# Optimization experiments

Hardware: AMD Instinct MI355X
Metric: run time of the kernel (lower is better)

Reference implementation:

```python
import jax, jax.numpy as jnp
import numpy as np

# Kernel offset table copied VERBATIM from the source (note the duplicated
# [-1,-1] row where [-1,1] would be expected -- we replicate the bug).
OFF = jnp.array([[-1, -1], [-1, 0], [-1, -1], [0, -1], [0, 0], [0, 1],
                 [1, -1], [1, 0], [1, 1]], dtype=jnp.float32)  # (9, 2)

T_HARD = 3.14 / 6
S_HARD = 2.0
S_RANGE = (S_HARD - 1.0 / S_HARD) / 2.0
H_VEC = jnp.array([T_HARD, S_RANGE, S_RANGE], dtype=jnp.float32)
B_VEC = jnp.array([0.0, S_RANGE, S_RANGE], dtype=jnp.float32)
BN_EPS = 1e-5


def setup_inputs() -> dict:
    key = jax.random.key(0)
    ks = jax.random.split(key, 9)
    N, C, H, W, O = 8, 128, 64, 64, 128
    return {
        "input_feat": jax.random.normal(ks[0], (N, C, H, W), jnp.float32),
        "ste_w": 0.05 * jax.random.normal(ks[1], (3, C, 1, 1), jnp.float32),
        "ste_b": 0.05 * jax.random.normal(ks[2], (3,), jnp.float32),
        "bn_gamma": 1.0 + 0.1 * jax.random.normal(ks[3], (3,), jnp.float32),
        "bn_beta": 0.1 * jax.random.normal(ks[4], (3,), jnp.float32),
        "bn_mean": 0.1 * jax.random.normal(ks[5], (3,), jnp.float32),
        "bn_var": jax.random.uniform(ks[6], (3,), jnp.float32, 0.5, 1.5),
        "dconv_w": jax.random.normal(ks[7], (O, C, 3, 3), jnp.float32) / np.sqrt(C * 9.0),
        "dconv_b": 0.05 * jax.random.normal(ks[8], (O,), jnp.float32),
    }


def _forward(input_feat, ste_w, ste_b, bn_gamma, bn_beta, bn_mean, bn_var,
             dconv_w, dconv_b):
    N, C, H, W = input_feat.shape
    O = dconv_w.shape[0]
    # --- ste: 1x1 conv -> BatchNorm (eval) -> tanh, then affine H*x + B ---
    s = jnp.einsum('nchw,oc->nohw', input_feat, ste_w[:, :, 0, 0])
    s = s + ste_b[None, :, None, None]
    scale = (bn_gamma / jnp.sqrt(bn_var + BN_EPS))
    s = (s - bn_mean[None, :, None, None]) * scale[None, :, None, None] \
        + bn_beta[None, :, None, None]
    info = jnp.tanh(s) * H_VEC[None, :, None, None] + B_VEC[None, :, None, None]
    # --- per-pixel 2x2 scaled rotation applied to kernel grid ---
    theta = info[:, 0]                  # [N,H,W]
    sin = jnp.sin(theta)
    cos = jnp.cos(theta)
    a00 = cos * info[:, 1]
    a11 = cos * info[:, 2]
    awt = jnp.stack([a00, -sin, sin, a11], axis=-1).reshape(N, H, W, 2, 2)
    offs = jnp.einsum('kd,nhwde->nkhwe', OFF, awt)   # [N,9,H,W,2]
    off_y = offs[..., 0]
    off_x = offs[..., 1]
    # --- deformable 3x3 conv, stride 1, padding 1, zero-pad bilinear ---
    k = jnp.arange(9)
    dy = (k // 3 - 1).astype(jnp.float32)  # default kernel y-offsets
    dx = (k % 3 - 1).astype(jnp.float32)
    yy = jnp.arange(H, dtype=jnp.float32)
    xx = jnp.arange(W, dtype=jnp.float32)
    y = yy[None, None, :, None] + dy[None, :, None, None] + off_y  # [N,9,H,W]
    x = xx[None, None, None, :] + dx[None, :, None, None] + off_x
    y0 = jnp.floor(y)
    x0 = jnp.floor(x)
    wy = y - y0
    wx = x - x0
    y0i = y0.astype(jnp.int32)
    x0i = x0.astype(jnp.int32)

    def gather(img, yi, xi):
        # img [C,H,W], yi/xi [9,H,W] -> [C,9,H,W], zero outside bounds
        valid = (yi >= 0) & (yi < H) & (xi >= 0) & (xi < W)
        v = img[:, jnp.clip(yi, 0, H - 1), jnp.clip(xi, 0, W - 1)]
        return v * valid[None].astype(img.dtype)

    def sample_one(img, y0i, x0i, wy, wx):
        v00 = gather(img, y0i, x0i)
        v01 = gather(img, y0i, x0i + 1)
        v10 = gather(img, y0i + 1, x0i)
        v11 = gather(img, y0i + 1, x0i + 1)
        return (v00 * ((1 - wy) * (1 - wx))[None]
                + v01 * ((1 - wy) * wx)[None]
                + v10 * (wy * (1 - wx))[None]
                + v11 * (wy * wx)[None])

    samp = jax.vmap(sample_one)(input_feat, y0i, x0i, wy, wx)  # [N,C,9,H,W]
    out = jnp.einsum('nckhw,ock->nohw', samp, dconv_w.reshape(O, C, 9))
    return out + dconv_b[None, :, None, None]


def reference(input_feat, ste_w, ste_b, bn_gamma, bn_beta, bn_mean, bn_var,
              dconv_w, dconv_b):
    return _forward(input_feat, ste_w, ste_b, bn_gamma, bn_beta, bn_mean,
                    bn_var, dconv_w, dconv_b)
```

## Files before the change

kernel.cpp:

```cpp
#include <hip/hip_runtime.h>

constexpr int kN = 8, kC = 128, kH = 64, kW = 64, kO = 128;
constexpr int kHW = kH * kW;

typedef float f32x4 __attribute__((ext_vector_type(4)));
typedef short bf16x8 __attribute__((ext_vector_type(8)));
typedef unsigned short ushort8 __attribute__((ext_vector_type(8)));

__device__ __forceinline__ float bf2f(unsigned short u) {
  unsigned int x = ((unsigned int)u) << 16;
  return __builtin_bit_cast(float, x);
}
__device__ __forceinline__ unsigned short f2bf(float f) {
  unsigned int b = __builtin_bit_cast(unsigned int, f);
  b += 0x7FFFu + ((b >> 16) & 1u);
  return (unsigned short)(b >> 16);
}

__global__ __launch_bounds__(256) void prep_kernel(
    const float* __restrict__ inp, const float* __restrict__ ste_w,
    const float* __restrict__ ste_b, const float* __restrict__ bn_g,
    const float* __restrict__ bn_b, const float* __restrict__ bn_m,
    const float* __restrict__ bn_v, unsigned short* __restrict__ nhwc,
    float* __restrict__ prm) {
  __shared__ float tile[kC * kW];
  __shared__ float part[4][3][kW];
  const int tid = threadIdx.x;
  const int nh = blockIdx.x;
  const int n = nh >> 6, h = nh & 63;
  const float* base = inp + (size_t)n * kC * kHW + h * kW;

  for (int i = tid; i < kC * kW; i += 256) {
    int c = i >> 6, w = i & 63;
    tile[i] = base[c * kHW + w];
  }
  __syncthreads();

  {
    const int w = tid & 63, cg = tid >> 6;
    float s0 = 0.f, s1 = 0.f, s2 = 0.f;
#pragma unroll 8
    for (int j = 0; j < 32; ++j) {
      int c = cg * 32 + j;
      float v = tile[c * kW + w];
      s0 += v * ste_w[c];
      s1 += v * ste_w[kC + c];
      s2 += v * ste_w[2 * kC + c];
    }
    part[cg][0][w] = s0;
    part[cg][1][w] = s1;
    part[cg][2][w] = s2;
  }
  __syncthreads();
  if (tid < kW) {
    const int w = tid;
    float s0 = part[0][0][w] + part[1][0][w] + part[2][0][w] + part[3][0][w];
    float s1 = part[0][1][w] + part[1][1][w] + part[2][1][w] + part[3][1][w];
    float s2 = part[0][2][w] + part[1][2][w] + part[2][2][w] + part[3][2][w];
    s0 = (s0 + ste_b[0] - bn_m[0]) * (bn_g[0] * rsqrtf(bn_v[0] + 1e-5f)) + bn_b[0];
    s1 = (s1 + ste_b[1] - bn_m[1]) * (bn_g[1] * rsqrtf(bn_v[1] + 1e-5f)) + bn_b[1];
    s2 = (s2 + ste_b[2] - bn_m[2]) * (bn_g[2] * rsqrtf(bn_v[2] + 1e-5f)) + bn_b[2];
    float th = tanhf(s0) * (3.14f / 6.0f);
    float i1 = tanhf(s1) * 0.75f + 0.75f;
    float i2 = tanhf(s2) * 0.75f + 0.75f;
    float sn = sinf(th), cs = cosf(th);
    prm[nh * 192 + w * 3 + 0] = cs * i1;
    prm[nh * 192 + w * 3 + 1] = sn;
    prm[nh * 192 + w * 3 + 2] = cs * i2;
  }

  for (int i = tid; i < kW * 16; i += 256) {
    int w = i & 63, ch = i >> 6;
    int c0 = ch * 8;
    ushort8 v;
#pragma unroll
    for (int j = 0; j < 8; ++j) v[j] = f2bf(tile[(c0 + j) * kW + w]);
    *(ushort8*)&nhwc[((size_t)(n * kH + h) * kW + w) * kC + c0] = v;
  }
}

__global__ __launch_bounds__(256) void reorder_bf16_kernel(
    const float* __restrict__ dw, unsigned short* __restrict__ wkb) {
  int idx = blockIdx.x * blockDim.x + threadIdx.x;
  if (idx >= 9 * kO * kC) return;
  int k = idx / (kO * kC);
  int r = idx - k * (kO * kC);
  int o = r >> 7, c = r & 127;
  wkb[idx] = f2bf(dw[(o * kC + c) * 9 + k]);
}

__global__ __launch_bounds__(512, 4) void deform_mfma_kernel(
    const unsigned short* __restrict__ nhwc,
    const unsigned short* __restrict__ wkb,
    const float* __restrict__ prm, const float* __restrict__ db,
    float* __restrict__ out) {
  __shared__ __align__(16) unsigned short As[2][32 * 128];
  __shared__ __align__(16) unsigned short Bs[2][128 * 128];

  const int tid = threadIdx.x;
  const int lane = tid & 63, wave = tid >> 6;
  const int nh = blockIdx.x >> 1;
  const int w0 = (blockIdx.x & 1) << 5;
  const int n = nh >> 6, h = nh & 63;
  const unsigned short* nhwc_n = nhwc + (size_t)n * kH * kW * kC;

  const int p = tid >> 4, ch = tid & 15;
  const float a00 = prm[nh * 192 + (w0 + p) * 3 + 0];
  const float sn  = prm[nh * 192 + (w0 + p) * 3 + 1];
  const float a11 = prm[nh * 192 + (w0 + p) * 3 + 2];

  const int mg = wave >> 2, ng = wave & 3;
  const int row = mg * 16 + (lane & 15);
  const int kq = lane >> 4;
  const int rsw = (row & 7) << 4;
  f32x4 acc[2];
  acc[0] = (f32x4){0.f, 0.f, 0.f, 0.f};
  acc[1] = (f32x4){0.f, 0.f, 0.f, 0.f};

  ushort8 bReg[4];
  ushort8 a00r, a01r, a10r, a11r;
  float w00, w01, w10, w11;

  auto issue_tap = [&](int k) {
    const unsigned short* wkp = wkb + (size_t)k * kO * kC;
#pragma unroll
    for (int it = 0; it < 4; ++it) {
      int i = tid + it * 512;
      int o = i >> 4, c8 = i & 15;
      bReg[it] = *(const ushort8*)&wkp[o * kC + c8 * 8];
    }
    const float fdy = (float)(k / 3 - 1);
    const float fdx = (float)(k % 3 - 1);
    const float o0 = fdy;
    const float o1 = (k == 2) ? -1.0f : fdx;
    float y = (float)h + fdy + o0 * a00 + o1 * sn;
    float x = (float)(w0 + p) + fdx - o0 * sn + o1 * a11;
    float y0f = floorf(y), x0f = floorf(x);
    float wy = y - y0f, wx = x - x0f;
    int y0 = (int)y0f, x0 = (int)x0f;
    bool yv0 = (unsigned)y0 < (unsigned)kH;
    bool yv1 = (unsigned)(y0 + 1) < (unsigned)kH;
    bool xv0 = (unsigned)x0 < (unsigned)kW;
    bool xv1 = (unsigned)(x0 + 1) < (unsigned)kW;
    int y0c = min(max(y0, 0), kH - 1);
    int y1c = min(max(y0 + 1, 0), kH - 1);
    int x0c = min(max(x0, 0), kW - 1);
    int x1c = min(max(x0 + 1, 0), kW - 1);
    w00 = (1.f - wy) * (1.f - wx) * (yv0 && xv0 ? 1.f : 0.f);
    w01 = (1.f - wy) * wx * (yv0 && xv1 ? 1.f : 0.f);
    w10 = wy * (1.f - wx) * (yv1 && xv0 ? 1.f : 0.f);
    w11 = wy * wx * (yv1 && xv1 ? 1.f : 0.f);
    const int cb = ch * 8;
    a00r = *(const ushort8*)&nhwc_n[((y0c * kW) + x0c) * kC + cb];
    a01r = *(const ushort8*)&nhwc_n[((y0c * kW) + x1c) * kC + cb];
    a10r = *(const ushort8*)&nhwc_n[((y1c * kW) + x0c) * kC + cb];
    a11r = *(const ushort8*)&nhwc_n[((y1c * kW) + x1c) * kC + cb];
  };

  auto write_tiles = [&](int buf) {
#pragma unroll
    for (int it = 0; it < 4; ++it) {
      int i = tid + it * 512;
      int o = i >> 4, c8 = i & 15;
      *(ushort8*)((char*)Bs[buf] + o * 256 + ((c8 * 16) ^ ((o & 7) << 4))) =
          bReg[it];
    }
    ushort8 r;
#pragma unroll
    for (int j = 0; j < 8; ++j) {
      float val = bf2f(a00r[j]) * w00 + bf2f(a01r[j]) * w01 +
                  bf2f(a10r[j]) * w10 + bf2f(a11r[j]) * w11;
      r[j] = f2bf(val);
    }
    *(ushort8*)((char*)As[buf] + p * 256 + ((ch * 16) ^ ((p & 7) << 4))) = r;
  };

  issue_tap(0);
  write_tiles(0);
  __syncthreads();

  for (int k = 0; k < 9; ++k) {
    const int cur = k & 1;
    if (k < 8) issue_tap(k + 1);

    const char* Ab = (const char*)As[cur];
    const char* Bb = (const char*)Bs[cur];
#pragma unroll
    for (int ks = 0; ks < 4; ++ks) {
      const int kb = ks * 64 + kq * 16;
      bf16x8 a = *(const bf16x8*)(Ab + row * 256 + (kb ^ rsw));
#pragma unroll
      for (int f = 0; f < 2; ++f) {
        const int orow = (ng * 2 + f) * 16 + (lane & 15);
        bf16x8 b = *(const bf16x8*)(Bb + orow * 256 + (kb ^ ((orow & 7) << 4)));
        acc[f] = __builtin_amdgcn_mfma_f32_16x16x32_bf16(a, b, acc[f], 0, 0, 0);
      }
    }

    if (k < 8) write_tiles(cur ^ 1);
    __syncthreads();
  }

  const int pixb = mg * 16 + (lane >> 4) * 4;
#pragma unroll
  for (int f = 0; f < 2; ++f) {
    const int o = (ng * 2 + f) * 16 + (lane & 15);
    const float bias = db[o];
    float4 v = {acc[f][0] + bias, acc[f][1] + bias, acc[f][2] + bias,
                acc[f][3] + bias};
    *(float4*)&out[((size_t)(n * kO + o)) * kHW + h * kW + w0 + pixb] = v;
  }
}

__global__ __launch_bounds__(256) void deform_kernel_f32(
    const float* __restrict__ inp, const float* __restrict__ ste_w,
    const float* __restrict__ ste_b, const float* __restrict__ bn_g,
    const float* __restrict__ bn_b, const float* __restrict__ bn_m,
    const float* __restrict__ bn_v, const float* __restrict__ dw,
    const float* __restrict__ db, float* __restrict__ out) {
  __shared__ __align__(16) float smp[kC * 16];
  __shared__ float prm[16][3];
  const int tid = threadIdx.x;
  const int base = blockIdx.x * 16;
  const int n = base / kHW;
  const int hw = base - n * kHW;
  const int h = hw / kW;
  const int w0 = hw - h * kW;
  const float* inp_n = inp + (size_t)n * kC * kHW;

  for (int i = tid; i < kC * 16; i += 256) {
    int c = i >> 4, p = i & 15;
    smp[i] = inp_n[c * kHW + h * kW + w0 + p];
  }
  __syncthreads();
  {
    const int p = tid >> 4, cl = tid & 15;
    float a0 = 0.f, a1 = 0.f, a2 = 0.f;
#pragma unroll
    for (int i = 0; i < 8; ++i) {
      int c = cl + (i << 4);
      float v = smp[c * 16 + p];
      a0 += v * ste_w[c];
      a1 += v * ste_w[kC + c];
      a2 += v * ste_w[2 * kC + c];
    }
#pragma unroll
    for (int off = 8; off; off >>= 1) {
      a0 += __shfl_down(a0, off, 16);
      a1 += __shfl_down(a1, off, 16);
      a2 += __shfl_down(a2, off, 16);
    }
    if (cl == 0) {
      float s0 = (a0 + ste_b[0] - bn_m[0]) * (bn_g[0] * rsqrtf(bn_v[0] + 1e-5f)) + bn_b[0];
      float s1 = (a1 + ste_b[1] - bn_m[1]) * (bn_g[1] * rsqrtf(bn_v[1] + 1e-5f)) + bn_b[1];
      float s2 = (a2 + ste_b[2] - bn_m[2]) * (bn_g[2] * rsqrtf(bn_v[2] + 1e-5f)) + bn_b[2];
      float th = tanhf(s0) * (3.14f / 6.0f);
      float i1 = tanhf(s1) * 0.75f + 0.75f;
      float i2 = tanhf(s2) * 0.75f + 0.75f;
      prm[p][0] = cosf(th) * i1;
      prm[p][1] = sinf(th);
      prm[p][2] = cosf(th) * i2;
    }
  }
  const int o = tid & 127;
  const int ph = tid >> 7;
  float acc[8] = {0.f};
  for (int k = 0; k < 9; ++k) {
    __syncthreads();
    const float fdy = (float)(k / 3 - 1);
    const float fdx = (float)(k % 3 - 1);
    const float o0 = fdy;
    const float o1 = (k == 2) ? -1.0f : fdx;
    for (int i = tid; i < kC * 16; i += 256) {
      int c = i >> 4, p = i & 15;
      float a00 = prm[p][0], sn = prm[p][1], a11 = prm[p][2];
      float y = (float)h + fdy + o0 * a00 + o1 * sn;
      float x = (float)(w0 + p) + fdx - o0 * sn + o1 * a11;
      float y0f = floorf(y), x0f = floorf(x);
      float wy = y - y0f, wx = x - x0f;
      int y0 = (int)y0f, x0 = (int)x0f;
      const float* ic = inp_n + c * kHW;
      bool yv0 = (unsigned)y0 < (unsigned)kH;
      bool yv1 = (unsigned)(y0 + 1) < (unsigned)kH;
      bool xv0 = (unsigned)x0 < (unsigned)kW;
      bool xv1 = (unsigned)(x0 + 1) < (unsigned)kW;
      int y0c = min(max(y0, 0), kH - 1);
      int y1c = min(max(y0 + 1, 0), kH - 1);
      int x0c = min(max(x0, 0), kW - 1);
      int x1c = min(max(x0 + 1, 0), kW - 1);
      float v00 = (yv0 && xv0) ? ic[y0c * kW + x0c] : 0.f;
      float v01 = (yv0 && xv1) ? ic[y0c * kW + x1c] : 0.f;
      float v10 = (yv1 && xv0) ? ic[y1c * kW + x0c] : 0.f;
      float v11 = (yv1 && xv1) ? ic[y1c * kW + x1c] : 0.f;
      smp[i] = v00 * (1.f - wy) * (1.f - wx) + v01 * (1.f - wy) * wx +
               v10 * wy * (1.f - wx) + v11 * wy * wx;
    }
    __syncthreads();
    const float* wp = dw + (size_t)o * kC * 9 + k;
#pragma unroll 4
    for (int c = 0; c < kC; ++c) {
      float wv = wp[(size_t)c * 9];
      const float4 s0 = *(const float4*)&smp[c * 16 + (ph << 3)];
      const float4 s1 = *(const float4*)&smp[c * 16 + (ph << 3) + 4];
      acc[0] += wv * s0.x; acc[1] += wv * s0.y; acc[2] += wv * s0.z; acc[3] += wv * s0.w;
      acc[4] += wv * s1.x; acc[5] += wv * s1.y; acc[6] += wv * s1.z; acc[7] += wv * s1.w;
    }
  }
  const float bias = db[o];
  float* op = out + ((size_t)(n * kO + o)) * kHW + h * kW + w0 + (ph << 3);
#pragma unroll
  for (int j = 0; j < 8; ++j) op[j] = acc[j] + bias;
}

extern "C" void kernel_launch(void* const* d_in, const int* in_sizes, int n_in,
                              void* d_out, int out_size, void* d_ws, size_t ws_size,
                              hipStream_t stream) {
  const float* inp   = (const float*)d_in[0];
  const float* ste_w = (const float*)d_in[1];
  const float* ste_b = (const float*)d_in[2];
  const float* bn_g  = (const float*)d_in[3];
  const float* bn_b  = (const float*)d_in[4];
  const float* bn_m  = (const float*)d_in[5];
  const float* bn_v  = (const float*)d_in[6];
  const float* dw    = (const float*)d_in[7];
  const float* db    = (const float*)d_in[8];
  float* out = (float*)d_out;

  const size_t nhwc_bytes = (size_t)kN * kH * kW * kC * 2;
  const size_t wkb_bytes = (size_t)9 * kO * kC * 2;
  const size_t prm_bytes = (size_t)kN * kH * kW * 3 * 4;
  const size_t need = nhwc_bytes + wkb_bytes + prm_bytes;

  if (ws_size >= need) {
    unsigned short* nhwc = (unsigned short*)d_ws;
    unsigned short* wkb = (unsigned short*)((char*)d_ws + nhwc_bytes);
    float* prm = (float*)((char*)d_ws + nhwc_bytes + wkb_bytes);
    prep_kernel<<<kN * kH, 256, 0, stream>>>(inp, ste_w, ste_b, bn_g, bn_b,
                                             bn_m, bn_v, nhwc, prm);
    int wtot = 9 * kO * kC;
    reorder_bf16_kernel<<<(wtot + 255) / 256, 256, 0, stream>>>(dw, wkb);
    deform_mfma_kernel<<<kN * kH * 2, 512, 0, stream>>>(nhwc, wkb, prm, db, out);
  } else {
    deform_kernel_f32<<<kN * kHW / 16, 256, 0, stream>>>(
        inp, ste_w, ste_b, bn_g, bn_b, bn_m, bn_v, dw, db, out);
  }
}
```

Baseline: 51.65 us.

## Merge weight reorder into prep kernel and use 64-pixel 32x32 MFMA tiles

The bf16 weight reorder moves into extra blocks of the prep kernel, which removes one kernel launch. The deform MFMA kernel now handles a full 64-pixel row per block instead of two 32-pixel halves, so each 128x128 weight tile loaded per tap is shared by twice as many pixels. It also switches from 16x16x32 to 32x32x16 MFMA tiles. This halves the number of blocks, doubles shared memory per block and lowers the occupancy hint from 4 to 2, which may reduce latency hiding for the gathers.

```diff
diff --git a/kernel.cpp b/kernel.cpp
--- a/kernel.cpp
+++ b/kernel.cpp
@@ -4,6 +4,7 @@
 constexpr int kHW = kH * kW;
 
 typedef float f32x4 __attribute__((ext_vector_type(4)));
+typedef float f32x16 __attribute__((ext_vector_type(16)));
 typedef short bf16x8 __attribute__((ext_vector_type(8)));
 typedef unsigned short ushort8 __attribute__((ext_vector_type(8)));
 
@@ -22,11 +23,24 @@
     const float* __restrict__ ste_b, const float* __restrict__ bn_g,
     const float* __restrict__ bn_b, const float* __restrict__ bn_m,
     const float* __restrict__ bn_v, unsigned short* __restrict__ nhwc,
-    float* __restrict__ prm) {
+    float* __restrict__ prm, const float* __restrict__ dw,
+    unsigned short* __restrict__ wkb) {
+  const int bid = blockIdx.x;
+  if (bid >= kN * kH) {
+    int idx = (bid - kN * kH) * 256 + threadIdx.x;
+    if (idx < 9 * kO * kC) {
+      int k = idx / (kO * kC);
+      int r = idx - k * (kO * kC);
+      int o = r >> 7, c = r & 127;
+      wkb[idx] = f2bf(dw[(o * kC + c) * 9 + k]);
+    }
+    return;
+  }
+
   __shared__ float tile[kC * kW];
   __shared__ float part[4][3][kW];
   const int tid = threadIdx.x;
-  const int nh = blockIdx.x;
+  const int nh = bid;
   const int n = nh >> 6, h = nh & 63;
   const float* base = inp + (size_t)n * kC * kHW + h * kW;
 
@@ -79,47 +93,45 @@
   }
 }
 
-__global__ __launch_bounds__(256) void reorder_bf16_kernel(
-    const float* __restrict__ dw, unsigned short* __restrict__ wkb) {
-  int idx = blockIdx.x * blockDim.x + threadIdx.x;
-  if (idx >= 9 * kO * kC) return;
-  int k = idx / (kO * kC);
-  int r = idx - k * (kO * kC);
-  int o = r >> 7, c = r & 127;
-  wkb[idx] = f2bf(dw[(o * kC + c) * 9 + k]);
-}
-
-__global__ __launch_bounds__(512, 4) void deform_mfma_kernel(
+__global__ __launch_bounds__(512, 2) void deform_mfma_kernel(
     const unsigned short* __restrict__ nhwc,
     const unsigned short* __restrict__ wkb,
     const float* __restrict__ prm, const float* __restrict__ db,
     float* __restrict__ out) {
-  __shared__ __align__(16) unsigned short As[2][32 * 128];
+  __shared__ __align__(16) unsigned short As[2][64 * 128];
   __shared__ __align__(16) unsigned short Bs[2][128 * 128];
 
   const int tid = threadIdx.x;
   const int lane = tid & 63, wave = tid >> 6;
-  const int nh = blockIdx.x >> 1;
-  const int w0 = (blockIdx.x & 1) << 5;
+  const int nh = blockIdx.x;
   const int n = nh >> 6, h = nh & 63;
   const unsigned short* nhwc_n = nhwc + (size_t)n * kH * kW * kC;
 
-  const int p = tid >> 4, ch = tid & 15;
-  const float a00 = prm[nh * 192 + (w0 + p) * 3 + 0];
-  const float sn  = prm[nh * 192 + (w0 + p) * 3 + 1];
-  const float a11 = prm[nh * 192 + (w0 + p) * 3 + 2];
+  const int p0 = tid >> 4, ch = tid & 15;
+  const int cb = ch * 8;
+  float a00[2], sn[2], a11[2];
+#pragma unroll
+  for (int it = 0; it < 2; ++it) {
+    const int w = p0 + it * 32;
+    a00[it] = prm[nh * 192 + w * 3 + 0];
+    sn[it]  = prm[nh * 192 + w * 3 + 1];
+    a11[it] = prm[nh * 192 + w * 3 + 2];
+  }
 
   const int mg = wave >> 2, ng = wave & 3;
-  const int row = mg * 16 + (lane & 15);
-  const int kq = lane >> 4;
-  const int rsw = (row & 7) << 4;
-  f32x4 acc[2];
-  acc[0] = (f32x4){0.f, 0.f, 0.f, 0.f};
-  acc[1] = (f32x4){0.f, 0.f, 0.f, 0.f};
+  const int arow = mg * 32 + (lane & 31);
+  const int brow = ng * 32 + (lane & 31);
+  const int koff = (lane >> 5) * 16;
+  const int aswz = (arow & 7) << 4;
+  const int bswz = (brow & 7) << 4;
+
+  f32x16 acc;
+#pragma unroll
+  for (int j = 0; j < 16; ++j) acc[j] = 0.f;
 
   ushort8 bReg[4];
-  ushort8 a00r, a01r, a10r, a11r;
-  float w00, w01, w10, w11;
+  ushort8 aC[2][4];
+  float wgt[2][4];
 
   auto issue_tap = [&](int k) {
     const unsigned short* wkp = wkb + (size_t)k * kO * kC;
@@ -133,28 +145,31 @@
     const float fdx = (float)(k % 3 - 1);
     const float o0 = fdy;
     const float o1 = (k == 2) ? -1.0f : fdx;
-    float y = (float)h + fdy + o0 * a00 + o1 * sn;
-    float x = (float)(w0 + p) + fdx - o0 * sn + o1 * a11;
-    float y0f = floorf(y), x0f = floorf(x);
-    float wy = y - y0f, wx = x - x0f;
-    int y0 = (int)y0f, x0 = (int)x0f;
-    bool yv0 = (unsigned)y0 < (unsigned)kH;
-    bool yv1 = (unsigned)(y0 + 1) < (unsigned)kH;
-    bool xv0 = (unsigned)x0 < (unsigned)kW;
-    bool xv1 = (unsigned)(x0 + 1) < (unsigned)kW;
-    int y0c = min(max(y0, 0), kH - 1);
-    int y1c = min(max(y0 + 1, 0), kH - 1);
-    int x0c = min(max(x0, 0), kW - 1);
-    int x1c = min(max(x0 + 1, 0), kW - 1);
-    w00 = (1.f - wy) * (1.f - wx) * (yv0 && xv0 ? 1.f : 0.f);
-    w01 = (1.f - wy) * wx * (yv0 && xv1 ? 1.f : 0.f);
-    w10 = wy * (1.f - wx) * (yv1 && xv0 ? 1.f : 0.f);
-    w11 = wy * wx * (yv1 && xv1 ? 1.f : 0.f);
-    const int cb = ch * 8;
-    a00r = *(const ushort8*)&nhwc_n[((y0c * kW) + x0c) * kC + cb];
-    a01r = *(const ushort8*)&nhwc_n[((y0c * kW) + x1c) * kC + cb];
-    a10r = *(const ushort8*)&nhwc_n[((y1c * kW) + x0c) * kC + cb];
-    a11r = *(const ushort8*)&nhwc_n[((y1c * kW) + x1c) * kC + cb];
+#pragma unroll
+    for (int it = 0; it < 2; ++it) {
+      const int p = p0 + it * 32;
+      float y = (float)h + fdy + o0 * a00[it] + o1 * sn[it];
+      float x = (float)p + fdx - o0 * sn[it] + o1 * a11[it];
+      float y0f = floorf(y), x0f = floorf(x);
+      float wy = y - y0f, wx = x - x0f;
+      int y0 = (int)y0f, x0 = (int)x0f;
+      bool yv0 = (unsigned)y0 < (unsigned)kH;
+      bool yv1 = (unsigned)(y0 + 1) < (unsigned)kH;
+      bool xv0 = (unsigned)x0 < (unsigned)kW;
+      bool xv1 = (unsigned)(x0 + 1) < (unsigned)kW;
+      int y0c = min(max(y0, 0), kH - 1);
+      int y1c = min(max(y0 + 1, 0), kH - 1);
+      int x0c = min(max(x0, 0), kW - 1);
+      int x1c = min(max(x0 + 1, 0), kW - 1);
+      wgt[it][0] = (1.f - wy) * (1.f - wx) * (yv0 && xv0 ? 1.f : 0.f);
+      wgt[it][1] = (1.f - wy) * wx * (yv0 && xv1 ? 1.f : 0.f);
+      wgt[it][2] = wy * (1.f - wx) * (yv1 && xv0 ? 1.f : 0.f);
+      wgt[it][3] = wy * wx * (yv1 && xv1 ? 1.f : 0.f);
+      aC[it][0] = *(const ushort8*)&nhwc_n[((y0c * kW) + x0c) * kC + cb];
+      aC[it][1] = *(const ushort8*)&nhwc_n[((y0c * kW) + x1c) * kC + cb];
+      aC[it][2] = *(const ushort8*)&nhwc_n[((y1c * kW) + x0c) * kC + cb];
+      aC[it][3] = *(const ushort8*)&nhwc_n[((y1c * kW) + x1c) * kC + cb];
+    }
   };
 
   auto write_tiles = [&](int buf) {
@@ -165,14 +180,20 @@
       *(ushort8*)((char*)Bs[buf] + o * 256 + ((c8 * 16) ^ ((o & 7) << 4))) =
           bReg[it];
     }
-    ushort8 r;
-#pragma unroll
-    for (int j = 0; j < 8; ++j) {
-      float val = bf2f(a00r[j]) * w00 + bf2f(a01r[j]) * w01 +
-                  bf2f(a10r[j]) * w10 + bf2f(a11r[j]) * w11;
-      r[j] = f2bf(val);
-    }
-    *(ushort8*)((char*)As[buf] + p * 256 + ((ch * 16) ^ ((p & 7) << 4))) = r;
+#pragma unroll
+    for (int it = 0; it < 2; ++it) {
+      const int p = p0 + it * 32;
+      ushort8 r;
+#pragma unroll
+      for (int j = 0; j < 8; ++j) {
+        float val = bf2f(aC[it][0][j]) * wgt[it][0] +
+                    bf2f(aC[it][1][j]) * wgt[it][1] +
+                    bf2f(aC[it][2][j]) * wgt[it][2] +
+                    bf2f(aC[it][3][j]) * wgt[it][3];
+        r[j] = f2bf(val);
+      }
+      *(ushort8*)((char*)As[buf] + p * 256 + ((ch * 16) ^ ((p & 7) << 4))) = r;
+    }
   };
 
   issue_tap(0);
@@ -183,32 +204,28 @@
     const int cur = k & 1;
     if (k < 8) issue_tap(k + 1);
 
-    const char* Ab = (const char*)As[cur];
-    const char* Bb = (const char*)Bs[cur];
-#pragma unroll
-    for (int ks = 0; ks < 4; ++ks) {
-      const int kb = ks * 64 + kq * 16;
-      bf16x8 a = *(const bf16x8*)(Ab + row * 256 + (kb ^ rsw));
-#pragma unroll
-      for (int f = 0; f < 2; ++f) {
-        const int orow = (ng * 2 + f) * 16 + (lane & 15);
-        bf16x8 b = *(const bf16x8*)(Bb + orow * 256 + (kb ^ ((orow & 7) << 4)));
-        acc[f] = __builtin_amdgcn_mfma_f32_16x16x32_bf16(a, b, acc[f], 0, 0, 0);
-      }
+    const char* Ab = (const char*)As[cur] + arow * 256;
+    const char* Bb = (const char*)Bs[cur] + brow * 256;
+#pragma unroll
+    for (int c = 0; c < 8; ++c) {
+      bf16x8 a = *(const bf16x8*)(Ab + ((c * 32 + koff) ^ aswz));
+      bf16x8 b = *(const bf16x8*)(Bb + ((c * 32 + koff) ^ bswz));
+      acc = __builtin_amdgcn_mfma_f32_32x32x16_bf16(a, b, acc, 0, 0, 0);
     }
 
     if (k < 8) write_tiles(cur ^ 1);
     __syncthreads();
   }
 
-  const int pixb = mg * 16 + (lane >> 4) * 4;
-#pragma unroll
-  for (int f = 0; f < 2; ++f) {
-    const int o = (ng * 2 + f) * 16 + (lane & 15);
-    const float bias = db[o];
-    float4 v = {acc[f][0] + bias, acc[f][1] + bias, acc[f][2] + bias,
-                acc[f][3] + bias};
-    *(float4*)&out[((size_t)(n * kO + o)) * kHW + h * kW + w0 + pixb] = v;
+  const int o = ng * 32 + (lane & 31);
+  const float bias = db[o];
+  float* obase = out + ((size_t)(n * kO + o)) * kHW + h * kW + mg * 32 +
+                 4 * (lane >> 5);
+#pragma unroll
+  for (int q = 0; q < 4; ++q) {
+    float4 v = {acc[4 * q + 0] + bias, acc[4 * q + 1] + bias,
+                acc[4 * q + 2] + bias, acc[4 * q + 3] + bias};
+    *(float4*)&obase[8 * q] = v;
   }
 }
 
@@ -335,11 +352,10 @@
     unsigned short* nhwc = (unsigned short*)d_ws;
     unsigned short* wkb = (unsigned short*)((char*)d_ws + nhwc_bytes);
     float* prm = (float*)((char*)d_ws + nhwc_bytes + wkb_bytes);
-    prep_kernel<<<kN * kH, 256, 0, stream>>>(inp, ste_w, ste_b, bn_g, bn_b,
-                                             bn_m, bn_v, nhwc, prm);
-    int wtot = 9 * kO * kC;
-    reorder_bf16_kernel<<<(wtot + 255) / 256, 256, 0, stream>>>(dw, wkb);
-    deform_mfma_kernel<<<kN * kH * 2, 512, 0, stream>>>(nhwc, wkb, prm, db, out);
+    const int reorder_blocks = (9 * kO * kC + 255) / 256;
+    prep_kernel<<<kN * kH + reorder_blocks, 256, 0, stream>>>(
+        inp, ste_w, ste_b, bn_g, bn_b, bn_m, bn_v, nhwc, prm, dw, wkb);
+    deform_mfma_kernel<<<kN * kH, 512, 0, stream>>>(nhwc, wkb, prm, db, out);
   } else {
     deform_kernel_f32<<<kN * kHW / 16, 256, 0, stream>>>(
         inp, ste_w, ste_b, bn_g, bn_b, bn_m, bn_v, dw, db, out);
```

Measured after the change: 52.89 us. 1.02x slower.
